# Performance work log

Hardware: AMD Instinct MI355X
Metric: run time of the kernel (lower is better)

## Reference

```python
import jax, jax.numpy as jnp
import numpy as np

DIM = 1024
NH = 16
HD = DIM // NH  # 64
NT = max(1, int(NH * 0.25))  # 4 time heads
NS = NH - NT                 # 12 space heads
SCALE = HD ** (-0.5)


def setup_inputs() -> dict:
    key = jax.random.key(0)
    ks = jax.random.split(key, 8)
    B, T = 2, 2048
    init = 0.02
    return {
        "x": jax.random.normal(ks[0], (B, T, DIM), dtype=jnp.float32),
        # weights stored as (in, out); torch Linear y = x @ W.T is equivalent
        "Wqt": jax.random.normal(ks[1], (DIM, NT * HD), dtype=jnp.float32) * init,
        "Wkt": jax.random.normal(ks[2], (DIM, NT * HD), dtype=jnp.float32) * init,
        "Wqs": jax.random.normal(ks[3], (DIM, NS * HD), dtype=jnp.float32) * init,
        "Wks": jax.random.normal(ks[4], (DIM, NS * HD), dtype=jnp.float32) * init,
        "Wv": jax.random.normal(ks[5], (DIM, DIM), dtype=jnp.float32) * init,
        "Wout": jax.random.normal(ks[6], (DIM, DIM), dtype=jnp.float32) * init,
        "bout": jnp.zeros((DIM,), dtype=jnp.float32),
        "w_sigma": jnp.zeros((1,), dtype=jnp.float32),
    }


def reference(x, Wqt, Wkt, Wqs, Wks, Wv, Wout, bout, w_sigma):
    B, T, D = x.shape
    Qt = (x @ Wqt).reshape(B, T, NT, HD)
    Kt = (x @ Wkt).reshape(B, T, NT, HD)
    Qs = (x @ Wqs).reshape(B, T, NS, HD)
    Ks = (x @ Wks).reshape(B, T, NS, HD)
    st = jnp.einsum('bthd,bshd->bths', Qt, Kt)  # [B,T,NT,T]
    ss = jnp.einsum('bthd,bshd->bths', Qs, Ks)  # [B,T,NS,T]
    sig = jax.nn.sigmoid(w_sigma)  # shape (1,), broadcasts
    score = jnp.concatenate([-sig * st, ss], axis=2) * SCALE  # [B,T,NH,T]
    attn = jax.nn.softmax(score, axis=-1)
    V = (x @ Wv).reshape(B, T, NH, HD)
    ctx = jnp.einsum('bths,bshd->bthd', attn, V).reshape(B, T, D)
    return ctx @ Wout + bout
```

## Files before the change

kernel.cpp:

```cpp
#include <hip/hip_runtime.h>
#include <hip/hip_bf16.h>

typedef __bf16 bf16_t;
typedef __bf16 bf16x4 __attribute__((ext_vector_type(4)));
typedef __bf16 bf16x8 __attribute__((ext_vector_type(8)));
typedef float  f32x4  __attribute__((ext_vector_type(4)));

#define DIM     1024
#define NHEAD   16
#define HDIM    64
#define NTIME   4
#define TSEQ    2048
#define NBATCH  2
#define SCALE_F 0.125f
#define LOG2E   1.4426950408889634f

#define GLL(gp, lp) __builtin_amdgcn_global_load_lds( \
    (const __attribute__((address_space(1))) unsigned int*)(const void*)(gp), \
    (__attribute__((address_space(3))) unsigned int*)(void*)(lp), 16, 0, 0)

#define OFF_WQKVT 0UL
#define OFF_WOUTT (OFF_WQKVT + 3072UL*1024UL*2UL)
#define OFF_Q     (OFF_WOUTT + 1024UL*1024UL*2UL)
#define OFF_K     (OFF_Q  + 2UL*16UL*2048UL*64UL*2UL)
#define OFF_VT    (OFF_K  + 2UL*16UL*2048UL*64UL*2UL)
#define OFF_CTX   (OFF_VT + 2UL*16UL*2048UL*64UL*2UL)

__global__ void prep_all(const float* __restrict__ x,
                         const float* __restrict__ Wqt, const float* __restrict__ Wkt,
                         const float* __restrict__ Wqs, const float* __restrict__ Wks,
                         const float* __restrict__ Wv,  const float* __restrict__ Wout,
                         bf16_t* __restrict__ Xb, bf16_t* __restrict__ WqkvT,
                         bf16_t* __restrict__ WoutT) {
    __shared__ float T[64][65];
    const int bid = blockIdx.x;
    if (bid < 2048) {
        int i = bid * 256 + threadIdx.x;
        const float4* s = (const float4*)(x + (size_t)i * 8);
        float4 a = s[0], b2 = s[1];
        bf16x8 v;
        v[0] = (bf16_t)a.x;  v[1] = (bf16_t)a.y;  v[2] = (bf16_t)a.z;  v[3] = (bf16_t)a.w;
        v[4] = (bf16_t)b2.x; v[5] = (bf16_t)b2.y; v[6] = (bf16_t)b2.z; v[7] = (bf16_t)b2.w;
        *(bf16x8*)(Xb + (size_t)i * 8) = v;
        return;
    }
    const int tc = threadIdx.x & 63, tr = threadIdx.x >> 6;
    if (bid < 2816) {
        const int l = bid - 2048;
        const int n0 = (l % 48) * 64;
        const int k0 = (l / 48) * 64;
        const int region = n0 >> 10;
        const int cc = n0 & 1023;
        const int h = cc >> 6;
        const float* src; int ncols, col0;
        if (region == 2) { src = Wv; ncols = 1024; col0 = cc; }
        else if (h < NTIME) { src = (region == 0) ? Wqt : Wkt; ncols = NTIME * HDIM; col0 = h * HDIM; }
        else                { src = (region == 0) ? Wqs : Wks; ncols = (NHEAD - NTIME) * HDIM; col0 = (h - NTIME) * HDIM; }
#pragma unroll
        for (int i = 0; i < 16; ++i) {
            int kl = tr * 16 + i;
            T[kl][tc] = src[(size_t)(k0 + kl) * ncols + col0 + tc];
        }
        __syncthreads();
#pragma unroll
        for (int i = 0; i < 16; ++i) {
            int nl = tr * 16 + i;
            WqkvT[(size_t)(n0 + nl) * 1024 + k0 + tc] = (bf16_t)T[tc][nl];
        }
    } else {
        const int l = bid - 2816;
        const int n0 = (l % 16) * 64;
        const int k0 = (l / 16) * 64;
#pragma unroll
        for (int i = 0; i < 16; ++i) {
            int kl = tr * 16 + i;
            T[kl][tc] = Wout[(size_t)(k0 + kl) * 1024 + n0 + tc];
        }
        __syncthreads();
#pragma unroll
        for (int i = 0; i < 16; ++i) {
            int nl = tr * 16 + i;
            WoutT[(size_t)(n0 + nl) * 1024 + k0 + tc] = (bf16_t)T[tc][nl];
        }
    }
}

template<int MODE, int NB>
__global__ __launch_bounds__(256)
void gemm_bf16(const bf16_t* __restrict__ Ab, const bf16_t* __restrict__ Bt,
               bf16_t* __restrict__ Qb, bf16_t* __restrict__ Kb, bf16_t* __restrict__ Vt,
               float* __restrict__ Cout, const float* __restrict__ bias)
{
    __shared__ __align__(16) bf16_t As[128][64];
    __shared__ __align__(16) bf16_t Bs[128][64];

    const int cpx = gridDim.x >> 3;
    const int l = (blockIdx.x & 7) * cpx + (blockIdx.x >> 3);
    const int m0 = (l / NB) * 128, n0 = (l % NB) * 128;

    const int tid  = threadIdx.x;
    const int lane = tid & 63;
    const int wave = tid >> 6;
    const int wm = (wave >> 1) * 64, wn = (wave & 1) * 64;
    const int g = lane >> 4, lr = lane & 15;

    f32x4 acc[4][4];
#pragma unroll
    for (int i = 0; i < 4; ++i)
#pragma unroll
        for (int j = 0; j < 4; ++j) acc[i][j] = f32x4{0.f, 0.f, 0.f, 0.f};

    for (int k0 = 0; k0 < 1024; k0 += 64) {
        __syncthreads();
#pragma unroll
        for (int c = 0; c < 4; ++c) {
            int idx  = tid + c * 256;
            int row  = idx >> 3;
            int csrc = (idx & 7) ^ (row & 7);
            GLL(Ab + (size_t)(m0 + row) * 1024 + k0 + csrc * 8,
                (char*)&As[0][0] + (c * 256 + wave * 64) * 16);
            GLL(Bt + (size_t)(n0 + row) * 1024 + k0 + csrc * 8,
                (char*)&Bs[0][0] + (c * 256 + wave * 64) * 16);
        }
        __syncthreads();

#pragma unroll
        for (int kk = 0; kk < 2; ++kk) {
            bf16x8 afr[4], bfr[4];
#pragma unroll
            for (int f = 0; f < 4; ++f) {
                int ra = wm + f * 16 + lr;
                afr[f] = *(const bf16x8*)((const char*)&As[0][0] + ra * 128 + (((kk * 4 + g) ^ (ra & 7)) << 4));
                int rb = wn + f * 16 + lr;
                bfr[f] = *(const bf16x8*)((const char*)&Bs[0][0] + rb * 128 + (((kk * 4 + g) ^ (rb & 7)) << 4));
            }
#pragma unroll
            for (int fm = 0; fm < 4; ++fm)
#pragma unroll
                for (int fn = 0; fn < 4; ++fn)
                    acc[fm][fn] = __builtin_amdgcn_mfma_f32_16x16x32_bf16(bfr[fn], afr[fm], acc[fm][fn], 0, 0, 0);
        }
    }

    const int region = n0 >> 10;
#pragma unroll
    for (int fm = 0; fm < 4; ++fm) {
        const int m = m0 + wm + fm * 16 + lr;
        const int b = m >> 11, t = m & 2047;
#pragma unroll
        for (int fn = 0; fn < 4; ++fn) {
            const int nb = n0 + wn + fn * 16 + g * 4;
            if constexpr (MODE == 1) {
                float4 bb = *(const float4*)(bias + nb);
                float4 v;
                v.x = acc[fm][fn][0] + bb.x;
                v.y = acc[fm][fn][1] + bb.y;
                v.z = acc[fm][fn][2] + bb.z;
                v.w = acc[fm][fn][3] + bb.w;
                *(float4*)(Cout + (size_t)m * DIM + nb) = v;
            } else {
                const int cc = nb & 1023;
                const int h = cc >> 6, d0 = cc & 63;
                const size_t bh = (size_t)(b * NHEAD + h);
                if (region == 2) {
#pragma unroll
                    for (int r = 0; r < 4; ++r)
                        Vt[(bh * HDIM + d0 + r) * TSEQ + t] = (bf16_t)acc[fm][fn][r];
                } else {
                    bf16x4 w;
#pragma unroll
                    for (int r = 0; r < 4; ++r) w[r] = (bf16_t)acc[fm][fn][r];
                    bf16_t* dst = (region == 0) ? Qb : Kb;
                    *(bf16x4*)(dst + (bh * TSEQ + t) * HDIM + d0) = w;
                }
            }
        }
    }
}

__global__ __launch_bounds__(256, 2)
void attn_kernel(const bf16_t* __restrict__ Qb, const bf16_t* __restrict__ Kb,
                 const bf16_t* __restrict__ Vt, bf16_t* __restrict__ ctx,
                 const float* __restrict__ w_sigma)
{
    __shared__ __align__(16) bf16_t Ktile[2][128][64];
    __shared__ __align__(16) bf16_t Vtile[2][64][128];
    __shared__ __align__(16) char   P2[4][4096];

    const int l    = ((blockIdx.x & 7) << 6) + (blockIdx.x >> 3);
    const int qc   = l & 15;
    const int bh   = l >> 4;
    const int h    = bh & 15;
    const int b    = bh >> 4;
    const int tid  = threadIdx.x;
    const int lane = tid & 63;
    const int wave = tid >> 6;
    const int g = lane >> 4, lr = lane & 15;
    const int q0 = qc * 128 + wave * 32;

    const float sig = 1.f / (1.f + __expf(-w_sigma[0]));
    const float fl2 = ((h < NTIME) ? (-sig * SCALE_F) : SCALE_F) * LOG2E;

    const bf16_t* Qp = Qb + (size_t)bh * TSEQ * HDIM;
    const bf16_t* Kp = Kb + (size_t)bh * TSEQ * HDIM;
    const bf16_t* Vp = Vt + (size_t)bh * HDIM * TSEQ;

    bf16x8 qa0 = *(const bf16x8*)(Qp + (size_t)(q0 + lr) * HDIM + g * 8);
    bf16x8 qa1 = *(const bf16x8*)(Qp + (size_t)(q0 + lr) * HDIM + 32 + g * 8);
    bf16x8 qb0 = *(const bf16x8*)(Qp + (size_t)(q0 + 16 + lr) * HDIM + g * 8);
    bf16x8 qb1 = *(const bf16x8*)(Qp + (size_t)(q0 + 16 + lr) * HDIM + 32 + g * 8);
#pragma unroll
    for (int e = 0; e < 8; ++e) {
        qa0[e] = (bf16_t)((float)qa0[e] * fl2);
        qa1[e] = (bf16_t)((float)qa1[e] * fl2);
        qb0[e] = (bf16_t)((float)qb0[e] * fl2);
        qb1[e] = (bf16_t)((float)qb1[e] * fl2);
    }

    f32x4 oA[4], oB[4];
#pragma unroll
    for (int n = 0; n < 4; ++n) { oA[n] = f32x4{0.f,0.f,0.f,0.f}; oB[n] = f32x4{0.f,0.f,0.f,0.f}; }
    float lpA = 0.f, lpB = 0.f;

    char* const P2w = &P2[wave][0];
    const int qsw = (lr & 7) << 4;

    const int krow = tid >> 3;
    const int kcg  = tid & 7;
    const int vrow = tid >> 4;
    const int vcg  = tid & 15;

    auto stage = [&](int s0, int buf) {
#pragma unroll
        for (int j = 0; j < 4; ++j) {
            int kr = j * 32 + krow;
            GLL(Kp + (size_t)(s0 + kr) * HDIM + ((kcg ^ (kr & 7)) << 3),
                (char*)&Ktile[buf][0][0] + (j * 256 + wave * 64) * 16);
            int vr = j * 16 + vrow;
            GLL(Vp + (size_t)vr * TSEQ + s0 + ((vcg ^ (vr & 15)) << 3),
                (char*)&Vtile[buf][0][0] + (j * 256 + wave * 64) * 16);
        }
    };

    auto half_compute = [&](const char* Kt, const char* Vc, int hf) {
        __builtin_amdgcn_s_setprio(1);
#pragma unroll
        for (int st = 0; st < 4; ++st) {
            const int srow = hf * 64 + st * 16 + lr;
            const int rs7 = lr & 7;
            bf16x8 kb0 = *(const bf16x8*)(Kt + srow * 128 + ((g ^ rs7) << 4));
            bf16x8 kb1 = *(const bf16x8*)(Kt + srow * 128 + (((4 + g) ^ rs7) << 4));
            f32x4 zA = f32x4{0.f,0.f,0.f,0.f}, zB = f32x4{0.f,0.f,0.f,0.f};
            zA = __builtin_amdgcn_mfma_f32_16x16x32_bf16(kb0, qa0, zA, 0, 0, 0);
            zA = __builtin_amdgcn_mfma_f32_16x16x32_bf16(kb1, qa1, zA, 0, 0, 0);
            zB = __builtin_amdgcn_mfma_f32_16x16x32_bf16(kb0, qb0, zB, 0, 0, 0);
            zB = __builtin_amdgcn_mfma_f32_16x16x32_bf16(kb1, qb1, zB, 0, 0, 0);
            float a0 = __builtin_amdgcn_exp2f(zA[0]);
            float a1 = __builtin_amdgcn_exp2f(zA[1]);
            float a2 = __builtin_amdgcn_exp2f(zA[2]);
            float a3 = __builtin_amdgcn_exp2f(zA[3]);
            float b0 = __builtin_amdgcn_exp2f(zB[0]);
            float b1 = __builtin_amdgcn_exp2f(zB[1]);
            float b2 = __builtin_amdgcn_exp2f(zB[2]);
            float b3 = __builtin_amdgcn_exp2f(zB[3]);
            bf16x4 wA, wB;
            wA[0] = (bf16_t)a0; wA[1] = (bf16_t)a1; wA[2] = (bf16_t)a2; wA[3] = (bf16_t)a3;
            wB[0] = (bf16_t)b0; wB[1] = (bf16_t)b1; wB[2] = (bf16_t)b2; wB[3] = (bf16_t)b3;
            *(bf16x4*)(P2w +        lr * 128 + ((st * 32 + g * 8) ^ qsw)) = wA;
            *(bf16x4*)(P2w + 2048 + lr * 128 + ((st * 32 + g * 8) ^ qsw)) = wB;
            lpA += (a0 + a1) + (a2 + a3);
            lpB += (b0 + b1) + (b2 + b3);
        }
        __builtin_amdgcn_s_setprio(0);

        asm volatile("s_waitcnt lgkmcnt(0)" ::: "memory");
        __builtin_amdgcn_sched_barrier(0);

        __builtin_amdgcn_s_setprio(1);
#pragma unroll
        for (int kc = 0; kc < 2; ++kc) {
            bf16x8 paA = *(const bf16x8*)(P2w +        lr * 128 + ((kc * 64 + g * 16) ^ qsw));
            bf16x8 paB = *(const bf16x8*)(P2w + 2048 + lr * 128 + ((kc * 64 + g * 16) ^ qsw));
#pragma unroll
            for (int n = 0; n < 4; ++n) {
                const int row = n * 16 + lr;
                bf16x8 vb = *(const bf16x8*)(Vc + row * 256 + (((hf * 8 + kc * 4 + g) ^ (row & 15)) << 4));
                oA[n] = __builtin_amdgcn_mfma_f32_16x16x32_bf16(vb, paA, oA[n], 0, 0, 0);
                oB[n] = __builtin_amdgcn_mfma_f32_16x16x32_bf16(vb, paB, oB[n], 0, 0, 0);
            }
        }
        __builtin_amdgcn_s_setprio(0);
    };

    const char* const K0 = (const char*)&Ktile[0][0][0];
    const char* const K1 = (const char*)&Ktile[1][0][0];
    const char* const V0 = (const char*)&Vtile[0][0][0];
    const char* const V1 = (const char*)&Vtile[1][0][0];

    stage(0, 0);
    __syncthreads();

    for (int it = 0; it < 8; ++it) {
        const int s0 = it * 256;
        stage(s0 + 128, 1);
        half_compute(K0, V0, 0);
        half_compute(K0, V0, 1);
        __syncthreads();
        if (s0 + 256 < TSEQ) stage(s0 + 256, 0);
        half_compute(K1, V1, 0);
        half_compute(K1, V1, 1);
        __syncthreads();
    }

    float lfA = lpA, lfB = lpB;
    lfA += __shfl_xor(lfA, 16, 64);
    lfA += __shfl_xor(lfA, 32, 64);
    lfB += __shfl_xor(lfB, 16, 64);
    lfB += __shfl_xor(lfB, 32, 64);
    float liA = 1.f / lfA, liB = 1.f / lfB;

    const int tA = q0 + lr, tB = q0 + 16 + lr;
#pragma unroll
    for (int n = 0; n < 4; ++n) {
        bf16x4 wA, wB;
#pragma unroll
        for (int r = 0; r < 4; ++r) {
            wA[r] = (bf16_t)(oA[n][r] * liA);
            wB[r] = (bf16_t)(oB[n][r] * liB);
        }
        *(bf16x4*)(ctx + ((size_t)(b * TSEQ + tA)) * DIM + h * HDIM + n * 16 + g * 4) = wA;
        *(bf16x4*)(ctx + ((size_t)(b * TSEQ + tB)) * DIM + h * HDIM + n * 16 + g * 4) = wB;
    }
}

extern "C" void kernel_launch(void* const* d_in, const int* in_sizes, int n_in,
                              void* d_out, int out_size, void* d_ws, size_t ws_size,
                              hipStream_t stream) {
    const float* x    = (const float*)d_in[0];
    const float* Wqt  = (const float*)d_in[1];
    const float* Wkt  = (const float*)d_in[2];
    const float* Wqs  = (const float*)d_in[3];
    const float* Wks  = (const float*)d_in[4];
    const float* Wv   = (const float*)d_in[5];
    const float* Wout = (const float*)d_in[6];
    const float* bout = (const float*)d_in[7];
    const float* wsig = (const float*)d_in[8];
    (void)in_sizes; (void)n_in; (void)out_size; (void)ws_size;

    char* ws = (char*)d_ws;
    bf16_t* WqkvT = (bf16_t*)(ws + OFF_WQKVT);
    bf16_t* WoutT = (bf16_t*)(ws + OFF_WOUTT);
    bf16_t* Qb    = (bf16_t*)(ws + OFF_Q);
    bf16_t* Kb    = (bf16_t*)(ws + OFF_K);
    bf16_t* Vt    = (bf16_t*)(ws + OFF_VT);
    bf16_t* ctx   = (bf16_t*)(ws + OFF_CTX);
    bf16_t* Xb    = ctx;
    float*  out   = (float*)d_out;

    prep_all<<<3072, 256, 0, stream>>>(x, Wqt, Wkt, Wqs, Wks, Wv, Wout, Xb, WqkvT, WoutT);

    gemm_bf16<0, 24><<<768, 256, 0, stream>>>(Xb, WqkvT, Qb, Kb, Vt, nullptr, nullptr);

    attn_kernel<<<512, 256, 0, stream>>>(Qb, Kb, Vt, ctx, wsig);

    gemm_bf16<1, 8><<<256, 256, 0, stream>>>(ctx, WoutT, nullptr, nullptr, nullptr, out, bout);
}
```

Baseline: 119.5 us.

## Shrink attention K/V tiles to 64 keys to fit three blocks per CU

Halves the staged K and V tiles from 128 to 64 keys per buffer, with matching swizzle changes, and rewrites the main loop as 32 double-buffered steps of 64 keys. Launch bounds rise to three blocks per SM/CU to use the freed LDS for occupancy. In exchange the kernel takes twice as many barriers per key sweep, and the register budget per thread tightens, which risks spills.

```diff
diff --git a/kernel.cpp b/kernel.cpp
--- a/kernel.cpp
+++ b/kernel.cpp
@@ -178,13 +178,13 @@
     }
 }
 
-__global__ __launch_bounds__(256, 2)
+__global__ __launch_bounds__(256, 3)
 void attn_kernel(const bf16_t* __restrict__ Qb, const bf16_t* __restrict__ Kb,
                  const bf16_t* __restrict__ Vt, bf16_t* __restrict__ ctx,
                  const float* __restrict__ w_sigma)
 {
-    __shared__ __align__(16) bf16_t Ktile[2][128][64];
-    __shared__ __align__(16) bf16_t Vtile[2][64][128];
+    __shared__ __align__(16) bf16_t Ktile[2][64][64];
+    __shared__ __align__(16) bf16_t Vtile[2][64][64];
     __shared__ __align__(16) char   P2[4][4096];
 
     const int l    = ((blockIdx.x & 7) << 6) + (blockIdx.x >> 3);
@@ -225,28 +225,26 @@
     char* const P2w = &P2[wave][0];
     const int qsw = (lr & 7) << 4;
 
-    const int krow = tid >> 3;
-    const int kcg  = tid & 7;
-    const int vrow = tid >> 4;
-    const int vcg  = tid & 15;
+    const int trow = tid >> 3;
+    const int tcg  = tid & 7;
 
     auto stage = [&](int s0, int buf) {
 #pragma unroll
-        for (int j = 0; j < 4; ++j) {
-            int kr = j * 32 + krow;
-            GLL(Kp + (size_t)(s0 + kr) * HDIM + ((kcg ^ (kr & 7)) << 3),
+        for (int j = 0; j < 2; ++j) {
+            int kr = j * 32 + trow;
+            GLL(Kp + (size_t)(s0 + kr) * HDIM + ((tcg ^ (kr & 7)) << 3),
                 (char*)&Ktile[buf][0][0] + (j * 256 + wave * 64) * 16);
-            int vr = j * 16 + vrow;
-            GLL(Vp + (size_t)vr * TSEQ + s0 + ((vcg ^ (vr & 15)) << 3),
+            int vr = j * 32 + trow;
+            GLL(Vp + (size_t)vr * TSEQ + s0 + ((tcg ^ (vr & 7)) << 3),
                 (char*)&Vtile[buf][0][0] + (j * 256 + wave * 64) * 16);
         }
     };
 
-    auto half_compute = [&](const char* Kt, const char* Vc, int hf) {
+    auto compute = [&](const char* Kt, const char* Vc) {
         __builtin_amdgcn_s_setprio(1);
 #pragma unroll
         for (int st = 0; st < 4; ++st) {
-            const int srow = hf * 64 + st * 16 + lr;
+            const int srow = st * 16 + lr;
             const int rs7 = lr & 7;
             bf16x8 kb0 = *(const bf16x8*)(Kt + srow * 128 + ((g ^ rs7) << 4));
             bf16x8 kb1 = *(const bf16x8*)(Kt + srow * 128 + (((4 + g) ^ rs7) << 4));
@@ -284,7 +282,7 @@
 #pragma unroll
             for (int n = 0; n < 4; ++n) {
                 const int row = n * 16 + lr;
-                bf16x8 vb = *(const bf16x8*)(Vc + row * 256 + (((hf * 8 + kc * 4 + g) ^ (row & 15)) << 4));
+                bf16x8 vb = *(const bf16x8*)(Vc + row * 128 + (((kc * 4 + g) ^ (row & 7)) << 4));
                 oA[n] = __builtin_amdgcn_mfma_f32_16x16x32_bf16(vb, paA, oA[n], 0, 0, 0);
                 oB[n] = __builtin_amdgcn_mfma_f32_16x16x32_bf16(vb, paB, oB[n], 0, 0, 0);
             }
@@ -300,15 +298,11 @@
     stage(0, 0);
     __syncthreads();
 
-    for (int it = 0; it < 8; ++it) {
-        const int s0 = it * 256;
-        stage(s0 + 128, 1);
-        half_compute(K0, V0, 0);
-        half_compute(K0, V0, 1);
-        __syncthreads();
-        if (s0 + 256 < TSEQ) stage(s0 + 256, 0);
-        half_compute(K1, V1, 0);
-        half_compute(K1, V1, 1);
+#pragma unroll 2
+    for (int step = 0; step < 32; ++step) {
+        const int cur = step & 1;
+        if (step < 31) stage((step + 1) * 64, cur ^ 1);
+        compute(cur ? K1 : K0, cur ? V1 : V0);
         __syncthreads();
     }
 
```

Measured after the change: 121.4 us. No clear change (+1.6%).
